# Performance work log

Measured on AMD Instinct MI355X. Metric: run time of the kernel, lower is better.

## Reference

```python
import jax, jax.numpy as jnp
import numpy as np

N_NODES = 50000
N_EDGES = 600000
IN_DIM = 128
HID = 256
OUT = 3


def setup_inputs() -> dict:
    key = jax.random.key(0)
    ks = jax.random.split(key, 10)
    x = jax.random.normal(ks[0], (N_NODES, IN_DIM), dtype=jnp.float32)
    edge_index = jax.random.randint(ks[1], (2, N_EDGES), 0, N_NODES, dtype=jnp.int64)
    s = lambda k, shp: jax.random.normal(k, shp, dtype=jnp.float32) * (1.0 / np.sqrt(shp[0]))
    return {
        "x": x,
        "edge_index": edge_index,
        # SAGEConv1: lin_l (applied to aggregated neighbors, with bias), lin_r (root, no bias)
        "W1l": s(ks[2], (IN_DIM, HID)), "b1": jnp.zeros((HID,), jnp.float32), "W1r": s(ks[3], (IN_DIM, HID)),
        # SAGEConv2
        "W2l": s(ks[4], (HID, HID)), "b2": jnp.zeros((HID,), jnp.float32), "W2r": s(ks[5], (HID, HID)),
        # classification head
        "Wh": s(ks[6], (HID, OUT)), "bh": jnp.zeros((OUT,), jnp.float32),
    }


def _sage_conv(x, edge_index, Wl, b, Wr):
    """PyG SAGEConv with mean aggregation: out = lin_l(mean_{j->i} x_j) + lin_r(x_i)."""
    src, dst = edge_index[0], edge_index[1]
    n = x.shape[0]
    # gather source features and scatter-mean onto targets
    msg_sum = jax.ops.segment_sum(x[src], dst, num_segments=n)          # [N, d]
    deg = jax.ops.segment_sum(jnp.ones((src.shape[0],), x.dtype), dst, num_segments=n)
    mean = msg_sum / jnp.maximum(deg, 1.0)[:, None]                      # isolated nodes -> 0
    return mean @ Wl + b + x @ Wr


def reference(x, edge_index, W1l, b1, W1r, W2l, b2, W2r, Wh, bh):
    h = jax.nn.relu(_sage_conv(x, edge_index, W1l, b1, W1r))
    # dropout(p=0.2) is identity in eval mode
    h = jax.nn.relu(_sage_conv(h, edge_index, W2l, b2, W2r))
    return h @ Wh + bh
```

## Files before the change

### kernel.cpp

```cpp
#include <hip/hip_runtime.h>
#include <hip/hip_bf16.h>

#define N_NODES 50000
#define N_EDGES 600000
#define IN_DIM 128
#define HID 256
#define OUT_DIM 3

#define M_PAD 50048

#define SCAN_B 256
#define SCAN_NB ((N_NODES + SCAN_B - 1) / SCAN_B)

#define XQ_SCALE (255.0f / 12.0f)
#define XQ_INV   (12.0f / 255.0f)
#define XQ_OFF   (-6.0f)
#define HQ_SCALE (255.0f / 8.0f)
#define HQ_INV   (8.0f / 255.0f)

typedef __bf16 bf16x8 __attribute__((ext_vector_type(8)));
typedef float f32x4 __attribute__((ext_vector_type(4)));

static __device__ __forceinline__ unsigned short f2b(float f) {
    union { float f; unsigned u; } u; u.f = f;
    unsigned r = u.u + 0x7fffu + ((u.u >> 16) & 1u);
    return (unsigned short)(r >> 16);
}
static __device__ __forceinline__ float b2f(unsigned short b) {
    union { unsigned u; float f; } u; u.u = ((unsigned)b) << 16;
    return u.f;
}


#define SETUP_CAST (N_NODES * IN_DIM / 4)
#define SETUP_T1 (SETUP_CAST + 196608)
#define SETUP_T2 (SETUP_T1 + N_NODES * 3)
#define SETUP_TOT (SETUP_T2 + N_EDGES)

__global__ __launch_bounds__(256) void setup_kernel(
    const float* __restrict__ x, unsigned short* __restrict__ xb, unsigned* __restrict__ xq,
    const float* __restrict__ W1l, const float* __restrict__ W1r,
    const float* __restrict__ W2l, const float* __restrict__ W2r,
    unsigned short* __restrict__ W1lt, unsigned short* __restrict__ W1rt,
    unsigned short* __restrict__ W2lt, unsigned short* __restrict__ W2rt,
    const float* __restrict__ bh, float* __restrict__ out,
    const int* __restrict__ dst, int* __restrict__ counts) {
    int i = blockIdx.x * blockDim.x + threadIdx.x;
    if (i < SETUP_CAST) {
        float4 v = ((const float4*)x)[i];
        ushort4 o;
        o.x = f2b(v.x); o.y = f2b(v.y); o.z = f2b(v.z); o.w = f2b(v.w);
        ((ushort4*)xb)[i] = o;
        float t0 = fminf(fmaxf((v.x - XQ_OFF) * XQ_SCALE, 0.f), 255.f);
        float t1 = fminf(fmaxf((v.y - XQ_OFF) * XQ_SCALE, 0.f), 255.f);
        float t2 = fminf(fmaxf((v.z - XQ_OFF) * XQ_SCALE, 0.f), 255.f);
        float t3 = fminf(fmaxf((v.w - XQ_OFF) * XQ_SCALE, 0.f), 255.f);
        unsigned q = (unsigned)(t0 + 0.5f) | ((unsigned)(t1 + 0.5f) << 8) |
                     ((unsigned)(t2 + 0.5f) << 16) | ((unsigned)(t3 + 0.5f) << 24);
        xq[i] = q;
    } else if (i < SETUP_T1) {
        int j = i - SETUP_CAST;
        const float* in; unsigned short* ow; int K;
        if (j < 32768)       { in = W1l; ow = W1lt; K = IN_DIM; }
        else if (j < 65536)  { in = W1r; ow = W1rt; K = IN_DIM; j -= 32768; }
        else if (j < 131072) { in = W2l; ow = W2lt; K = HID;    j -= 65536; }
        else                 { in = W2r; ow = W2rt; K = HID;    j -= 131072; }
        int k = j >> 8;
        int n = j & 255;
        ow[(size_t)n * K + k] = f2b(in[j]);
    } else if (i < SETUP_T2) {
        int j = i - SETUP_T1;
        out[j] = bh[j % 3];
    } else if (i < SETUP_TOT) {
        int e = i - SETUP_T2;
        atomicAdd(&counts[dst[e]], 1);
    }
}


__global__ __launch_bounds__(256) void block_sum_kernel(const int* __restrict__ counts,
                                                        int* __restrict__ partial) {
    int node = blockIdx.x * SCAN_B + threadIdx.x;
    int v = (node < N_NODES) ? counts[node] : 0;
#pragma unroll
    for (int off = 32; off > 0; off >>= 1) v += __shfl_down(v, off);
    __shared__ int ws[4];
    if ((threadIdx.x & 63) == 0) ws[threadIdx.x >> 6] = v;
    __syncthreads();
    if (threadIdx.x == 0) partial[blockIdx.x] = ws[0] + ws[1] + ws[2] + ws[3];
}

__global__ __launch_bounds__(256) void write_rowptr_kernel(const int* __restrict__ counts,
                                                           const int* __restrict__ partial,
                                                           int* __restrict__ row_ptr) {
    __shared__ int s[SCAN_B];
    __shared__ int wsum[4];
    int t = threadIdx.x;
    int pv = (t < blockIdx.x && t < SCAN_NB) ? partial[t] : 0;
#pragma unroll
    for (int off = 32; off > 0; off >>= 1) pv += __shfl_down(pv, off);
    if ((t & 63) == 0) wsum[t >> 6] = pv;
    __syncthreads();
    int base = wsum[0] + wsum[1] + wsum[2] + wsum[3];
    int node = blockIdx.x * SCAN_B + t;
    int v = (node < N_NODES) ? counts[node] : 0;
    s[t] = v;
    __syncthreads();
    for (int off = 1; off < SCAN_B; off <<= 1) {
        int u = (t >= off) ? s[t - off] : 0;
        __syncthreads();
        s[t] += u;
        __syncthreads();
    }
    if (node < N_NODES) row_ptr[node] = base + s[t] - v;
    if (node == 0) row_ptr[N_NODES] = N_EDGES;
}

__global__ void fill_csr_kernel(const int* __restrict__ src, const int* __restrict__ dst,
                                const int* __restrict__ row_ptr, int* __restrict__ cursor,
                                int* __restrict__ csr_src) {
    int e = blockIdx.x * blockDim.x + threadIdx.x;
    if (e < N_EDGES) {
        int d = dst[e];
        int pos = atomicAdd(&cursor[d], 1);
        csr_src[row_ptr[d] + pos] = src[e];
    }
}


static __device__ __forceinline__ void addb(unsigned* acc, uint4 v) {
    acc[0]  += v.x & 0xff; acc[1]  += (v.x >> 8) & 0xff; acc[2]  += (v.x >> 16) & 0xff; acc[3]  += v.x >> 24;
    acc[4]  += v.y & 0xff; acc[5]  += (v.y >> 8) & 0xff; acc[6]  += (v.y >> 16) & 0xff; acc[7]  += v.y >> 24;
    acc[8]  += v.z & 0xff; acc[9]  += (v.z >> 8) & 0xff; acc[10] += (v.z >> 16) & 0xff; acc[11] += v.z >> 24;
    acc[12] += v.w & 0xff; acc[13] += (v.w >> 8) & 0xff; acc[14] += (v.w >> 16) & 0xff; acc[15] += v.w >> 24;
}

static __device__ __forceinline__ uint4 pack8(const float* a) {
    uint4 pk;
    pk.x = (unsigned)f2b(a[0]) | ((unsigned)f2b(a[1]) << 16);
    pk.y = (unsigned)f2b(a[2]) | ((unsigned)f2b(a[3]) << 16);
    pk.z = (unsigned)f2b(a[4]) | ((unsigned)f2b(a[5]) << 16);
    pk.w = (unsigned)f2b(a[6]) | ((unsigned)f2b(a[7]) << 16);
    return pk;
}

__global__ __launch_bounds__(256) void agg_mean256_u8_kernel(const unsigned char* __restrict__ featq,
                                                             const int* __restrict__ row_ptr,
                                                             const int* __restrict__ csr_src,
                                                             unsigned short* __restrict__ out) {
    int node = blockIdx.x * 4 + (threadIdx.x >> 6);
    if (node >= N_NODES) return;
    int lane = threadIdx.x & 63;
    int g = lane >> 4, lq = lane & 15;
    const uint4* f = (const uint4*)featq;
    unsigned acc[16];
#pragma unroll
    for (int j = 0; j < 16; j++) acc[j] = 0u;
    int beg = row_ptr[node], end = row_ptr[node + 1];
    int i = beg;
    for (; i + 16 <= end; i += 16) {
        int s0 = csr_src[i + g];
        int s1 = csr_src[i + 4 + g];
        int s2 = csr_src[i + 8 + g];
        int s3 = csr_src[i + 12 + g];
        uint4 v0 = f[(size_t)s0 * 16 + lq];
        uint4 v1 = f[(size_t)s1 * 16 + lq];
        uint4 v2 = f[(size_t)s2 * 16 + lq];
        uint4 v3 = f[(size_t)s3 * 16 + lq];
        addb(acc, v0); addb(acc, v1); addb(acc, v2); addb(acc, v3);
    }
    int r = end - i;
    int rem = r & 3;
    int tb = i + (r & ~3);
    bool tl = g < rem;
    uint4 u0, u1, u2, ut;
    if (r >= 4)  { int s = csr_src[i + g];     u0 = f[(size_t)s * 16 + lq]; }
    if (r >= 8)  { int s = csr_src[i + 4 + g]; u1 = f[(size_t)s * 16 + lq]; }
    if (r >= 12) { int s = csr_src[i + 8 + g]; u2 = f[(size_t)s * 16 + lq]; }
    if (tl)      { int s = csr_src[tb + g];    ut = f[(size_t)s * 16 + lq]; }
    if (r >= 4)  addb(acc, u0);
    if (r >= 8)  addb(acc, u1);
    if (r >= 12) addb(acc, u2);
    if (tl) addb(acc, ut);
#pragma unroll
    for (int j = 0; j < 16; j++) {
        acc[j] += (unsigned)__shfl_xor((int)acc[j], 32);
        acc[j] += (unsigned)__shfl_xor((int)acc[j], 16);
    }
    float inv = (end > beg) ? HQ_INV / (float)(end - beg) : 0.0f;
    if (g == 0) {
        float m[16];
#pragma unroll
        for (int j = 0; j < 16; j++) m[j] = (float)acc[j] * inv;
        uint4* orow = (uint4*)(out + (size_t)node * 256);
        orow[lq * 2]     = pack8(m);
        orow[lq * 2 + 1] = pack8(m + 8);
    }
}

__global__ __launch_bounds__(256) void agg_mean128_u8_kernel(const unsigned char* __restrict__ featq,
                                                             const int* __restrict__ row_ptr,
                                                             const int* __restrict__ csr_src,
                                                             unsigned short* __restrict__ out) {
    int node = blockIdx.x * 4 + (threadIdx.x >> 6);
    if (node >= N_NODES) return;
    int lane = threadIdx.x & 63;
    int g = lane >> 3, lq = lane & 7;
    const uint4* f = (const uint4*)featq;
    unsigned acc[16];
#pragma unroll
    for (int j = 0; j < 16; j++) acc[j] = 0u;
    int beg = row_ptr[node], end = row_ptr[node + 1];
    int i = beg;
    for (; i + 16 <= end; i += 16) {
        int s0 = csr_src[i + g];
        int s1 = csr_src[i + 8 + g];
        uint4 v0 = f[(size_t)s0 * 8 + lq];
        uint4 v1 = f[(size_t)s1 * 8 + lq];
        addb(acc, v0); addb(acc, v1);
    }
    int r = end - i;
    int rem = r & 7;
    int tb = i + (r & ~7);
    bool tl = g < rem;
    uint4 u0, ut;
    if (r >= 8) { int s = csr_src[i + g];  u0 = f[(size_t)s * 8 + lq]; }
    if (tl)     { int s = csr_src[tb + g]; ut = f[(size_t)s * 8 + lq]; }
    if (r >= 8) addb(acc, u0);
    if (tl) addb(acc, ut);
#pragma unroll
    for (int j = 0; j < 16; j++) {
        acc[j] += (unsigned)__shfl_xor((int)acc[j], 32);
        acc[j] += (unsigned)__shfl_xor((int)acc[j], 16);
        acc[j] += (unsigned)__shfl_xor((int)acc[j], 8);
    }
    bool has = end > beg;
    float inv = has ? XQ_INV / (float)(end - beg) : 0.0f;
    float o = has ? XQ_OFF : 0.0f;
    if (g == 0) {
        float m[16];
#pragma unroll
        for (int j = 0; j < 16; j++) m[j] = (float)acc[j] * inv + o;
        uint4* orow = (uint4*)(out + (size_t)node * 128);
        orow[lq * 2]     = pack8(m);
        orow[lq * 2 + 1] = pack8(m + 8);
    }
}


template <int KP>
static __device__ __forceinline__ void gemm_pipe_loop(
    const unsigned short* __restrict__ A0, const unsigned short* __restrict__ W0t,
    const unsigned short* __restrict__ A1, const unsigned short* __restrict__ W1t,
    unsigned short* As, unsigned short* Bs,
    int m0, int n0, int t, int w, int quad, int lr, f32x4 (&acc)[8]) {
    constexpr int KI = KP / 32;
    constexpr int NIT = 2 * KI;
    const int kb = t & 3;
    const int r  = t >> 2;
    const int rs = r ^ (kb << 2);
    const int lrs = lr ^ (quad << 2);

    const unsigned short* Aa[2] = {A0, A1};
    const unsigned short* Wa[2] = {W0t, W1t};

    uint4 ra0, rb0, rb1;
    auto gload = [&](int it) {
        int p = it / KI;
        int k0 = (it % KI) * 32 + kb * 8;
        const unsigned short* A = Aa[p];
        const unsigned short* Wt = Wa[p];
        ra0 = *(const uint4*)(A + (size_t)(m0 + r) * KP + k0);
        rb0 = *(const uint4*)(Wt + (size_t)(n0 + r) * KP + k0);
        rb1 = *(const uint4*)(Wt + (size_t)(n0 + 64 + r) * KP + k0);
    };
    auto wlds = [&](int buf) {
        unsigned short* pa = As + buf * 2048;
        unsigned short* pb = Bs + buf * 4096;
        *(uint4*)&pa[(kb * 64 + rs) * 8] = ra0;
        *(uint4*)&pb[(kb * 128 + rs) * 8] = rb0;
        *(uint4*)&pb[(kb * 128 + 64 + rs) * 8] = rb1;
    };

    gload(0);
    wlds(0);
    __syncthreads();
    for (int it = 0; it < NIT; ++it) {
        if (it + 1 < NIT) gload(it + 1);
        const unsigned short* pa = As + (it & 1) * 2048;
        const unsigned short* pb = Bs + (it & 1) * 4096;
        bf16x8 a0, b[8];
        a0 = *(const bf16x8*)&pa[(quad * 64 + w * 16 + lrs) * 8];
#pragma unroll
        for (int nt = 0; nt < 8; nt++)
            b[nt] = *(const bf16x8*)&pb[(quad * 128 + nt * 16 + lrs) * 8];
#pragma unroll
        for (int nt = 0; nt < 8; nt++)
            acc[nt] = __builtin_amdgcn_mfma_f32_16x16x32_bf16(a0, b[nt], acc[nt], 0, 0, 0);
        if (it + 1 < NIT) {
            wlds((it + 1) & 1);
            __syncthreads();
        }
    }
}

template <int KP>
__global__ __launch_bounds__(256) void gemm_pipe_kernel(
    const unsigned short* __restrict__ A0, const unsigned short* __restrict__ W0t,
    const unsigned short* __restrict__ A1, const unsigned short* __restrict__ W1t,
    const float* __restrict__ bias, unsigned short* __restrict__ out,
    unsigned char* __restrict__ outq, int M) {
    __shared__ __align__(16) unsigned short As[2 * 2048];
    __shared__ __align__(16) unsigned short Bs[2 * 4096];

    const int t = threadIdx.x;
    const int w = t >> 6, l = t & 63;
    const int quad = l >> 4, lr = l & 15;
    const int m0 = blockIdx.x * 64, n0 = blockIdx.y * 128;

    f32x4 acc[8];
    const f32x4 zero = {0.f, 0.f, 0.f, 0.f};
#pragma unroll
    for (int nt = 0; nt < 8; nt++) acc[nt] = zero;

    float bias_r[8];
#pragma unroll
    for (int nt = 0; nt < 8; nt++) bias_r[nt] = bias[n0 + nt * 16 + lr];

    gemm_pipe_loop<KP>(A0, W0t, A1, W1t, As, Bs, m0, n0, t, w, quad, lr, acc);

#pragma unroll
    for (int r = 0; r < 4; r++) {
        int gm = m0 + w * 16 + quad * 4 + r;
        if (gm >= M) continue;
#pragma unroll
        for (int nt = 0; nt < 8; nt++) {
            int col = n0 + nt * 16 + lr;
            float v = fmaxf(acc[nt][r] + bias_r[nt], 0.f);
            out[(size_t)gm * HID + col] = f2b(v);
            outq[(size_t)gm * HID + col] = (unsigned char)(fminf(v * HQ_SCALE, 255.f) + 0.5f);
        }
    }
}

template <int KP>
__global__ __launch_bounds__(256) void gemm_pipe_head_kernel(
    const unsigned short* __restrict__ A0, const unsigned short* __restrict__ W0t,
    const unsigned short* __restrict__ A1, const unsigned short* __restrict__ W1t,
    const float* __restrict__ bias, const float* __restrict__ Wh,
    float* __restrict__ out, int M) {
    __shared__ __align__(16) unsigned short As[2 * 2048];
    __shared__ __align__(16) unsigned short Bs[2 * 4096];

    const int t = threadIdx.x;
    const int w = t >> 6, l = t & 63;
    const int quad = l >> 4, lr = l & 15;
    const int m0 = blockIdx.x * 64, n0 = blockIdx.y * 128;

    f32x4 acc[8];
    const f32x4 zero = {0.f, 0.f, 0.f, 0.f};
#pragma unroll
    for (int nt = 0; nt < 8; nt++) acc[nt] = zero;

    float bias_r[8];
    float wh_r[8][3];
#pragma unroll
    for (int nt = 0; nt < 8; nt++) {
        int gn = n0 + nt * 16 + lr;
        bias_r[nt] = bias[gn];
        wh_r[nt][0] = Wh[gn * 3 + 0];
        wh_r[nt][1] = Wh[gn * 3 + 1];
        wh_r[nt][2] = Wh[gn * 3 + 2];
    }

    gemm_pipe_loop<KP>(A0, W0t, A1, W1t, As, Bs, m0, n0, t, w, quad, lr, acc);

#pragma unroll
    for (int r = 0; r < 4; r++) {
        int gm = m0 + w * 16 + quad * 4 + r;
        float p0 = 0.f, p1 = 0.f, p2 = 0.f;
#pragma unroll
        for (int nt = 0; nt < 8; nt++) {
            float v = fmaxf(acc[nt][r] + bias_r[nt], 0.f);
            p0 += v * wh_r[nt][0];
            p1 += v * wh_r[nt][1];
            p2 += v * wh_r[nt][2];
        }
#pragma unroll
        for (int off = 1; off < 16; off <<= 1) {
            p0 += __shfl_xor(p0, off);
            p1 += __shfl_xor(p1, off);
            p2 += __shfl_xor(p2, off);
        }
        if (lr == 0 && gm < M) {
            atomicAdd(&out[(size_t)gm * 3 + 0], p0);
            atomicAdd(&out[(size_t)gm * 3 + 1], p1);
            atomicAdd(&out[(size_t)gm * 3 + 2], p2);
        }
    }
}


extern "C" void kernel_launch(void* const* d_in, const int* in_sizes, int n_in,
                              void* d_out, int out_size, void* d_ws, size_t ws_size,
                              hipStream_t stream) {
    const float* x   = (const float*)d_in[0];
    const int*   ei  = (const int*)d_in[1];
    const int*   src = ei;
    const int*   dst = ei + N_EDGES;
    const float* W1l = (const float*)d_in[2];
    const float* b1  = (const float*)d_in[3];
    const float* W1r = (const float*)d_in[4];
    const float* W2l = (const float*)d_in[5];
    const float* b2  = (const float*)d_in[6];
    const float* W2r = (const float*)d_in[7];
    const float* Wh  = (const float*)d_in[8];
    const float* bh  = (const float*)d_in[9];
    float* out = (float*)d_out;

    char* ws = (char*)d_ws;
    size_t off = 0;
    auto alloc = [&](size_t bytes) -> void* {
        void* p = ws + off;
        off = (off + bytes + 255) & ~(size_t)255;
        return p;
    };
    int* counts   = (int*)alloc((size_t)N_NODES * 4);
    int* row_ptr  = (int*)alloc((size_t)(N_NODES + 1) * 4);
    int* cursor   = (int*)alloc((size_t)N_NODES * 4);
    int* partial  = (int*)alloc((size_t)SCAN_NB * 4);
    int* csr_src  = (int*)alloc((size_t)N_EDGES * 4);
    unsigned short* xb   = (unsigned short*)alloc((size_t)M_PAD * IN_DIM * 2);
    unsigned short* agg  = (unsigned short*)alloc((size_t)M_PAD * HID * 2);
    unsigned short* h1   = (unsigned short*)alloc((size_t)M_PAD * HID * 2);
    unsigned short* W1lt = (unsigned short*)alloc((size_t)IN_DIM * HID * 2);
    unsigned short* W1rt = (unsigned short*)alloc((size_t)IN_DIM * HID * 2);
    unsigned short* W2lt = (unsigned short*)alloc((size_t)HID * HID * 2);
    unsigned short* W2rt = (unsigned short*)alloc((size_t)HID * HID * 2);
    unsigned*       xq   = (unsigned*)alloc((size_t)N_NODES * IN_DIM);
    unsigned char*  h1q  = (unsigned char*)alloc((size_t)M_PAD * HID);

    hipMemsetAsync(counts, 0, (size_t)N_NODES * 4, stream);
    hipMemsetAsync(cursor, 0, (size_t)N_NODES * 4, stream);

    setup_kernel<<<(SETUP_TOT + 255) / 256, 256, 0, stream>>>(
        x, xb, xq, W1l, W1r, W2l, W2r, W1lt, W1rt, W2lt, W2rt, bh, out, dst, counts);

    const int eblocks = (N_EDGES + 255) / 256;
    block_sum_kernel<<<SCAN_NB, SCAN_B, 0, stream>>>(counts, partial);
    write_rowptr_kernel<<<SCAN_NB, SCAN_B, 0, stream>>>(counts, partial, row_ptr);
    fill_csr_kernel<<<eblocks, 256, 0, stream>>>(src, dst, row_ptr, cursor, csr_src);

    const int nblocks4 = (N_NODES + 3) / 4;
    dim3 gg(M_PAD / 64, HID / 128);

    agg_mean128_u8_kernel<<<nblocks4, 256, 0, stream>>>((const unsigned char*)xq, row_ptr, csr_src, agg);
    gemm_pipe_kernel<IN_DIM><<<gg, 256, 0, stream>>>(agg, W1lt, xb, W1rt, b1, h1, h1q, N_NODES);

    agg_mean256_u8_kernel<<<nblocks4, 256, 0, stream>>>(h1q, row_ptr, csr_src, agg);
    gemm_pipe_head_kernel<HID><<<gg, 256, 0, stream>>>(agg, W2lt, h1, W2rt, b2, Wh, out, N_NODES);
}
```

Baseline: 270.3 us.

## Deepen GEMM prefetch pipeline to triple-buffered LDS with register staging

Replaces the double-buffered LDS GEMM main loop with a three-stage scheme. Global loads are issued three iterations ahead into rotating register slots, and each slot is written to LDS one iteration before use. The full __syncthreads is replaced by an LDS-only waitcnt plus a raw barrier, so outstanding global loads are not drained at each step. This costs more VGPRs for the staged loads and 50% more shared memory per block, which may reduce occupancy. Indexing the register arrays with % 3 could also force them into scratch if the loop is not fully unrolled.

```diff
diff --git a/kernel.cpp b/kernel.cpp
--- a/kernel.cpp
+++ b/kernel.cpp
@@ -264,31 +264,38 @@
     const unsigned short* Aa[2] = {A0, A1};
     const unsigned short* Wa[2] = {W0t, W1t};
 
-    uint4 ra0, rb0, rb1;
+    uint4 ra[3], rb0[3], rb1[3];
     auto gload = [&](int it) {
+        int s = it % 3;
         int p = it / KI;
         int k0 = (it % KI) * 32 + kb * 8;
         const unsigned short* A = Aa[p];
         const unsigned short* Wt = Wa[p];
-        ra0 = *(const uint4*)(A + (size_t)(m0 + r) * KP + k0);
-        rb0 = *(const uint4*)(Wt + (size_t)(n0 + r) * KP + k0);
-        rb1 = *(const uint4*)(Wt + (size_t)(n0 + 64 + r) * KP + k0);
+        ra[s]  = *(const uint4*)(A + (size_t)(m0 + r) * KP + k0);
+        rb0[s] = *(const uint4*)(Wt + (size_t)(n0 + r) * KP + k0);
+        rb1[s] = *(const uint4*)(Wt + (size_t)(n0 + 64 + r) * KP + k0);
     };
-    auto wlds = [&](int buf) {
-        unsigned short* pa = As + buf * 2048;
-        unsigned short* pb = Bs + buf * 4096;
-        *(uint4*)&pa[(kb * 64 + rs) * 8] = ra0;
-        *(uint4*)&pb[(kb * 128 + rs) * 8] = rb0;
-        *(uint4*)&pb[(kb * 128 + 64 + rs) * 8] = rb1;
+    auto wlds = [&](int it) {
+        int b = it % 3;
+        unsigned short* pa = As + b * 2048;
+        unsigned short* pb = Bs + b * 4096;
+        *(uint4*)&pa[(kb * 64 + rs) * 8] = ra[b];
+        *(uint4*)&pb[(kb * 128 + rs) * 8] = rb0[b];
+        *(uint4*)&pb[(kb * 128 + 64 + rs) * 8] = rb1[b];
     };
 
     gload(0);
     wlds(0);
-    __syncthreads();
+    gload(1);
+    gload(2);
+    asm volatile("s_waitcnt lgkmcnt(0)" ::: "memory");
+    __builtin_amdgcn_s_barrier();
+
     for (int it = 0; it < NIT; ++it) {
-        if (it + 1 < NIT) gload(it + 1);
-        const unsigned short* pa = As + (it & 1) * 2048;
-        const unsigned short* pb = Bs + (it & 1) * 4096;
+        if (it + 1 < NIT) wlds(it + 1);
+        if (it + 3 < NIT) gload(it + 3);
+        const unsigned short* pa = As + (it % 3) * 2048;
+        const unsigned short* pb = Bs + (it % 3) * 4096;
         bf16x8 a0, b[8];
         a0 = *(const bf16x8*)&pa[(quad * 64 + w * 16 + lrs) * 8];
 #pragma unroll
@@ -298,8 +305,8 @@
         for (int nt = 0; nt < 8; nt++)
             acc[nt] = __builtin_amdgcn_mfma_f32_16x16x32_bf16(a0, b[nt], acc[nt], 0, 0, 0);
         if (it + 1 < NIT) {
-            wlds((it + 1) & 1);
-            __syncthreads();
+            asm volatile("s_waitcnt lgkmcnt(0)" ::: "memory");
+            __builtin_amdgcn_s_barrier();
         }
     }
 }
@@ -310,8 +317,8 @@
     const unsigned short* __restrict__ A1, const unsigned short* __restrict__ W1t,
     const float* __restrict__ bias, unsigned short* __restrict__ out,
     unsigned char* __restrict__ outq, int M) {
-    __shared__ __align__(16) unsigned short As[2 * 2048];
-    __shared__ __align__(16) unsigned short Bs[2 * 4096];
+    __shared__ __align__(16) unsigned short As[3 * 2048];
+    __shared__ __align__(16) unsigned short Bs[3 * 4096];
 
     const int t = threadIdx.x;
     const int w = t >> 6, l = t & 63;
@@ -349,8 +356,8 @@
     const unsigned short* __restrict__ A1, const unsigned short* __restrict__ W1t,
     const float* __restrict__ bias, const float* __restrict__ Wh,
     float* __restrict__ out, int M) {
-    __shared__ __align__(16) unsigned short As[2 * 2048];
-    __shared__ __align__(16) unsigned short Bs[2 * 4096];
+    __shared__ __align__(16) unsigned short As[3 * 2048];
+    __shared__ __align__(16) unsigned short Bs[3 * 4096];
 
     const int t = threadIdx.x;
     const int w = t >> 6, l = t & 63;
```

Result: no change. 273.0 us (+1.0%).
